# Kernel optimization log

Measured on AMD Instinct MI355X. Metric: run time of the kernel, lower is better.

The kernel has to match this reference:

```python
import jax, jax.numpy as jnp
import numpy as np

WINDOW = 32  # hardcoded in module; half-window = 16

def _final_mask(T):
    # sparse local window |i-j| <= 16 AND causal j <= i  =>  0 <= i-j <= 16
    i = jnp.arange(T)[:, None]
    j = jnp.arange(T)[None, :]
    d = i - j
    return (d >= 0) & (d <= WINDOW // 2)  # [T, T] bool

def setup_inputs() -> dict:
    key = jax.random.key(0)
    k1, k2, k3, k4 = jax.random.split(key, 4)
    B, T, C, H = 2, 8192, 1024, 64
    x = jax.random.normal(k1, (B, T, C), dtype=jnp.float32)
    Wq = jax.random.normal(k2, (C, H), dtype=jnp.float32) * (1.0 / np.sqrt(C))
    Wk = jax.random.normal(k3, (C, H), dtype=jnp.float32) * (1.0 / np.sqrt(C))
    Wv = jax.random.normal(k4, (C, H), dtype=jnp.float32) * (1.0 / np.sqrt(C))
    return {"x": x, "Wq": Wq, "Wk": Wk, "Wv": Wv}

def reference(x, Wq, Wk, Wv):
    B, T, C = x.shape
    H = Wq.shape[1]
    scale = jnp.sqrt(jnp.float32(H))
    q = jnp.einsum('btc,ch->bth', x, Wq)
    k = jnp.einsum('btc,ch->bth', x, Wk)
    v = jnp.einsum('btc,ch->bth', x, Wv)
    scores = jnp.einsum('bth,bsh->bts', q, k) / scale  # [B, T, T]
    mask = _final_mask(T)  # [T, T]
    scores = jnp.where(mask[None, :, :], scores, -jnp.inf)
    attn = jax.nn.softmax(scores, axis=-1)  # dropout is identity in eval mode
    out = jnp.einsum('bts,bsh->bth', attn, v)  # [B, T, H]
    return out
```

## Files before the change

kernel.cpp:

```cpp
#include <hip/hip_runtime.h>

typedef __bf16 bf16x8 __attribute__((ext_vector_type(8)));
typedef float f32x4 __attribute__((ext_vector_type(4)));

#define T_SEQ 8192
#define NB 2
#define CDIM 1024
#define HDIM 64
#define NROWS (NB * T_SEQ)

static __device__ __forceinline__ unsigned short f2b(float f) {
    union { float f; unsigned u; } a; a.f = f;
    unsigned r = a.u + 0x7FFFu + ((a.u >> 16) & 1u);
    return (unsigned short)(r >> 16);
}

__global__ __launch_bounds__(256) void wt_kernel(const float* __restrict__ Wq,
                                                 const float* __restrict__ Wk,
                                                 const float* __restrict__ Wv,
                                                 unsigned short* __restrict__ WT) {
    int idx = blockIdx.x * 256 + threadIdx.x;
    int m   = idx >> 16;
    int rem = idx & 65535;
    int n = rem >> 10, k = rem & 1023;
    const float* W = (m == 0) ? Wq : (m == 1) ? Wk : Wv;
    WT[idx] = f2b(W[k * HDIM + n]);
}

__global__ __launch_bounds__(256) void qkv_kernel(const float* __restrict__ x,
                                                  const unsigned short* __restrict__ WT,
                                                  float* __restrict__ q,
                                                  float* __restrict__ k,
                                                  float* __restrict__ v) {
    __shared__ unsigned short Al[32][72];
    __shared__ unsigned short Bl[192][72];

    int tid  = threadIdx.x;
    int lane = tid & 63;
    int w    = tid >> 6;
    int lr   = lane & 15, lg = lane >> 4;
    long row0 = (long)blockIdx.x * 32;

    f32x4 acc[2][3];
    #pragma unroll
    for (int mi = 0; mi < 2; ++mi)
        #pragma unroll
        for (int ni = 0; ni < 3; ++ni)
            acc[mi][ni] = (f32x4){0.f, 0.f, 0.f, 0.f};

    int ar = tid >> 3, aq = tid & 7;
    const float* xr = x + (row0 + ar) * CDIM;

    for (int kt = 0; kt < CDIM; kt += 64) {
        float4 f0 = ((const float4*)(xr + kt))[aq];
        float4 f1 = ((const float4*)(xr + kt))[aq + 8];
        ushort4 u0, u1;
        u0.x = f2b(f0.x); u0.y = f2b(f0.y); u0.z = f2b(f0.z); u0.w = f2b(f0.w);
        u1.x = f2b(f1.x); u1.y = f2b(f1.y); u1.z = f2b(f1.z); u1.w = f2b(f1.w);
        *(ushort4*)&Al[ar][aq * 4]      = u0;
        *(ushort4*)&Al[ar][32 + aq * 4] = u1;

        #pragma unroll
        for (int i = 0; i < 6; ++i) {
            int wi = tid + i * 256;
            int r = wi >> 3, ch = wi & 7;
            uint4 val = *(const uint4*)(WT + r * CDIM + kt + ch * 8);
            *(uint4*)&Bl[r][ch * 8] = val;
        }
        __syncthreads();

        #pragma unroll
        for (int kk = 0; kk < 2; ++kk) {
            bf16x8 a0 = *(const bf16x8*)&Al[lr][kk * 32 + lg * 8];
            bf16x8 a1 = *(const bf16x8*)&Al[16 + lr][kk * 32 + lg * 8];
            bf16x8 b0 = *(const bf16x8*)&Bl[w * 48 + lr][kk * 32 + lg * 8];
            bf16x8 b1 = *(const bf16x8*)&Bl[w * 48 + 16 + lr][kk * 32 + lg * 8];
            bf16x8 b2 = *(const bf16x8*)&Bl[w * 48 + 32 + lr][kk * 32 + lg * 8];
            acc[0][0] = __builtin_amdgcn_mfma_f32_16x16x32_bf16(a0, b0, acc[0][0], 0, 0, 0);
            acc[1][0] = __builtin_amdgcn_mfma_f32_16x16x32_bf16(a1, b0, acc[1][0], 0, 0, 0);
            acc[0][1] = __builtin_amdgcn_mfma_f32_16x16x32_bf16(a0, b1, acc[0][1], 0, 0, 0);
            acc[1][1] = __builtin_amdgcn_mfma_f32_16x16x32_bf16(a1, b1, acc[1][1], 0, 0, 0);
            acc[0][2] = __builtin_amdgcn_mfma_f32_16x16x32_bf16(a0, b2, acc[0][2], 0, 0, 0);
            acc[1][2] = __builtin_amdgcn_mfma_f32_16x16x32_bf16(a1, b2, acc[1][2], 0, 0, 0);
        }
        __syncthreads();
    }

    #pragma unroll
    for (int mi = 0; mi < 2; ++mi)
        #pragma unroll
        for (int ni = 0; ni < 3; ++ni) {
            int cg  = w * 48 + ni * 16 + lr;
            int mat = cg >> 6, cc = cg & 63;
            float* op = (mat == 0) ? q : (mat == 1) ? k : v;
            long rbase = row0 + mi * 16 + lg * 4;
            #pragma unroll
            for (int j = 0; j < 4; ++j)
                op[(rbase + j) * HDIM + cc] = acc[mi][ni][j];
        }
}

#define DOT4(a, b) ((a).x*(b).x + (a).y*(b).y + (a).z*(b).z + (a).w*(b).w)

__global__ __launch_bounds__(256) void attn_kernel(const float* __restrict__ q,
                                                   const float* __restrict__ k,
                                                   const float* __restrict__ v,
                                                   float* __restrict__ out) {
    __shared__ float Kl[80][68];
    __shared__ float Vl[80][68];
    __shared__ float Ql[64][68];

    int tid = threadIdx.x;
    int b   = blockIdx.y;
    int r0  = blockIdx.x * 64;
    const float* qb = q + (long)b * T_SEQ * HDIM;
    const float* kb = k + (long)b * T_SEQ * HDIM;
    const float* vb = v + (long)b * T_SEQ * HDIM;

    #pragma unroll
    for (int i = 0; i < 5; ++i) {
        int f = tid + i * 256;
        int r = f >> 4, c = (f & 15) * 4;
        int gr = r0 - 16 + r; if (gr < 0) gr = 0;
        *(float4*)&Kl[r][c] = *(const float4*)(kb + (long)gr * HDIM + c);
        *(float4*)&Vl[r][c] = *(const float4*)(vb + (long)gr * HDIM + c);
    }
    #pragma unroll
    for (int i = 0; i < 4; ++i) {
        int f = tid + i * 256;
        int r = f >> 4, c = (f & 15) * 4;
        *(float4*)&Ql[r][c] = *(const float4*)(qb + (long)(r0 + r) * HDIM + c);
    }
    __syncthreads();

    int r = tid >> 2, p = tid & 3;
    int i_row = r0 + r;

    float4 q0 = *(float4*)&Ql[r][p * 16 + 0];
    float4 q1 = *(float4*)&Ql[r][p * 16 + 4];
    float4 q2 = *(float4*)&Ql[r][p * 16 + 8];
    float4 q3 = *(float4*)&Ql[r][p * 16 + 12];

    float s[17];
    float mx = -1e30f;
    #pragma unroll
    for (int jj = 0; jj < 17; ++jj) {
        float d;
        if (i_row - 16 + jj < 0) {
            d = -1e30f;
        } else {
            const float* kr = &Kl[r + jj][p * 16];
            float4 k0 = *(const float4*)(kr + 0);
            float4 k1 = *(const float4*)(kr + 4);
            float4 k2 = *(const float4*)(kr + 8);
            float4 k3 = *(const float4*)(kr + 12);
            float pd = DOT4(q0, k0) + DOT4(q1, k1) + DOT4(q2, k2) + DOT4(q3, k3);
            pd += __shfl_xor(pd, 1, 64);
            pd += __shfl_xor(pd, 2, 64);
            d = pd * 0.125f;
        }
        s[jj] = d;
        mx = fmaxf(mx, d);
    }

    float denom = 0.f;
    float4 o0 = {0,0,0,0}, o1 = {0,0,0,0}, o2 = {0,0,0,0}, o3 = {0,0,0,0};
    #pragma unroll
    for (int jj = 0; jj < 17; ++jj) {
        float wgt = expf(s[jj] - mx);
        denom += wgt;
        const float* vr = &Vl[r + jj][p * 16];
        float4 v0 = *(const float4*)(vr + 0);
        float4 v1 = *(const float4*)(vr + 4);
        float4 v2 = *(const float4*)(vr + 8);
        float4 v3 = *(const float4*)(vr + 12);
        o0.x += wgt * v0.x; o0.y += wgt * v0.y; o0.z += wgt * v0.z; o0.w += wgt * v0.w;
        o1.x += wgt * v1.x; o1.y += wgt * v1.y; o1.z += wgt * v1.z; o1.w += wgt * v1.w;
        o2.x += wgt * v2.x; o2.y += wgt * v2.y; o2.z += wgt * v2.z; o2.w += wgt * v2.w;
        o3.x += wgt * v3.x; o3.y += wgt * v3.y; o3.z += wgt * v3.z; o3.w += wgt * v3.w;
    }
    float inv = 1.f / denom;
    o0.x *= inv; o0.y *= inv; o0.z *= inv; o0.w *= inv;
    o1.x *= inv; o1.y *= inv; o1.z *= inv; o1.w *= inv;
    o2.x *= inv; o2.y *= inv; o2.z *= inv; o2.w *= inv;
    o3.x *= inv; o3.y *= inv; o3.z *= inv; o3.w *= inv;

    float* ob = out + ((long)b * T_SEQ + i_row) * HDIM + p * 16;
    *(float4*)&ob[0]  = o0;
    *(float4*)&ob[4]  = o1;
    *(float4*)&ob[8]  = o2;
    *(float4*)&ob[12] = o3;
}

extern "C" void kernel_launch(void* const* d_in, const int* in_sizes, int n_in,
                              void* d_out, int out_size, void* d_ws, size_t ws_size,
                              hipStream_t stream) {
    const float* x  = (const float*)d_in[0];
    const float* Wq = (const float*)d_in[1];
    const float* Wk = (const float*)d_in[2];
    const float* Wv = (const float*)d_in[3];
    float* out = (float*)d_out;

    unsigned short* WT = (unsigned short*)d_ws;
    float* qws = (float*)((char*)d_ws + 393216);
    float* kws = qws + (long)NROWS * HDIM;
    float* vws = kws + (long)NROWS * HDIM;

    wt_kernel<<<dim3(768), dim3(256), 0, stream>>>(Wq, Wk, Wv, WT);
    qkv_kernel<<<dim3(NROWS / 32), dim3(256), 0, stream>>>(x, WT, qws, kws, vws);
    attn_kernel<<<dim3(T_SEQ / 64, NB), dim3(256), 0, stream>>>(qws, kws, vws, out);
}
```

Before: 125.6 us.

## Drop LDS staging in QKV GEMM and attention; load operands directly from global

The QKV projection kernel no longer stages x and W tiles in shared memory with block barriers. Each wave computes 16 rows by all 192 output columns, reading bf16 weight fragments directly from global/L2 and software-prefetching the next x slice. The attention kernel reads Q, K and V straight from global memory instead of copying a window into LDS, skips masked rows, and uses fast __expf. This removes LDS traffic and synchronization, but it relies on cache hits for the redundant weight and K/V reads across waves and gives up LDS reuse.

Result: slower. 200.0 us (+59.3%).

```diff
diff --git a/kernel.cpp b/kernel.cpp
--- a/kernel.cpp
+++ b/kernel.cpp
@@ -13,6 +13,13 @@
     union { float f; unsigned u; } a; a.f = f;
     unsigned r = a.u + 0x7FFFu + ((a.u >> 16) & 1u);
     return (unsigned short)(r >> 16);
+}
+
+static __device__ __forceinline__ bf16x8 pack8(float4 a, float4 b) {
+    union { bf16x8 v; unsigned short u[8]; } r;
+    r.u[0] = f2b(a.x); r.u[1] = f2b(a.y); r.u[2] = f2b(a.z); r.u[3] = f2b(a.w);
+    r.u[4] = f2b(b.x); r.u[5] = f2b(b.y); r.u[6] = f2b(b.z); r.u[7] = f2b(b.w);
+    return r.v;
 }
 
 __global__ __launch_bounds__(256) void wt_kernel(const float* __restrict__ Wq,
@@ -32,72 +39,45 @@
                                                   float* __restrict__ q,
                                                   float* __restrict__ k,
                                                   float* __restrict__ v) {
-    __shared__ unsigned short Al[32][72];
-    __shared__ unsigned short Bl[192][72];
-
     int tid  = threadIdx.x;
     int lane = tid & 63;
     int w    = tid >> 6;
     int lr   = lane & 15, lg = lane >> 4;
-    long row0 = (long)blockIdx.x * 32;
+    long r0  = ((long)blockIdx.x * 4 + w) * 16;
 
-    f32x4 acc[2][3];
+    const float* xrow = x + (r0 + lr) * CDIM + lg * 8;
+    const unsigned short* bbase = WT + (long)lr * CDIM + lg * 8;
+
+    f32x4 acc[12];
     #pragma unroll
-    for (int mi = 0; mi < 2; ++mi)
+    for (int ni = 0; ni < 12; ++ni) acc[ni] = (f32x4){0.f, 0.f, 0.f, 0.f};
+
+    float4 c0 = *(const float4*)(xrow + 0);
+    float4 c1 = *(const float4*)(xrow + 4);
+
+    for (int ks = 0; ks < CDIM; ks += 32) {
+        int kn = (ks + 32) & (CDIM - 1);
+        float4 n0 = *(const float4*)(xrow + kn + 0);
+        float4 n1 = *(const float4*)(xrow + kn + 4);
+        bf16x8 af = pack8(c0, c1);
         #pragma unroll
-        for (int ni = 0; ni < 3; ++ni)
-            acc[mi][ni] = (f32x4){0.f, 0.f, 0.f, 0.f};
-
-    int ar = tid >> 3, aq = tid & 7;
-    const float* xr = x + (row0 + ar) * CDIM;
-
-    for (int kt = 0; kt < CDIM; kt += 64) {
-        float4 f0 = ((const float4*)(xr + kt))[aq];
-        float4 f1 = ((const float4*)(xr + kt))[aq + 8];
-        ushort4 u0, u1;
-        u0.x = f2b(f0.x); u0.y = f2b(f0.y); u0.z = f2b(f0.z); u0.w = f2b(f0.w);
-        u1.x = f2b(f1.x); u1.y = f2b(f1.y); u1.z = f2b(f1.z); u1.w = f2b(f1.w);
-        *(ushort4*)&Al[ar][aq * 4]      = u0;
-        *(ushort4*)&Al[ar][32 + aq * 4] = u1;
-
-        #pragma unroll
-        for (int i = 0; i < 6; ++i) {
-            int wi = tid + i * 256;
-            int r = wi >> 3, ch = wi & 7;
-            uint4 val = *(const uint4*)(WT + r * CDIM + kt + ch * 8);
-            *(uint4*)&Bl[r][ch * 8] = val;
+        for (int ni = 0; ni < 12; ++ni) {
+            bf16x8 bf = *(const bf16x8*)(bbase + ni * 16 * CDIM + ks);
+            acc[ni] = __builtin_amdgcn_mfma_f32_16x16x32_bf16(af, bf, acc[ni], 0, 0, 0);
         }
-        __syncthreads();
-
-        #pragma unroll
-        for (int kk = 0; kk < 2; ++kk) {
-            bf16x8 a0 = *(const bf16x8*)&Al[lr][kk * 32 + lg * 8];
-            bf16x8 a1 = *(const bf16x8*)&Al[16 + lr][kk * 32 + lg * 8];
-            bf16x8 b0 = *(const bf16x8*)&Bl[w * 48 + lr][kk * 32 + lg * 8];
-            bf16x8 b1 = *(const bf16x8*)&Bl[w * 48 + 16 + lr][kk * 32 + lg * 8];
-            bf16x8 b2 = *(const bf16x8*)&Bl[w * 48 + 32 + lr][kk * 32 + lg * 8];
-            acc[0][0] = __builtin_amdgcn_mfma_f32_16x16x32_bf16(a0, b0, acc[0][0], 0, 0, 0);
-            acc[1][0] = __builtin_amdgcn_mfma_f32_16x16x32_bf16(a1, b0, acc[1][0], 0, 0, 0);
-            acc[0][1] = __builtin_amdgcn_mfma_f32_16x16x32_bf16(a0, b1, acc[0][1], 0, 0, 0);
-            acc[1][1] = __builtin_amdgcn_mfma_f32_16x16x32_bf16(a1, b1, acc[1][1], 0, 0, 0);
-            acc[0][2] = __builtin_amdgcn_mfma_f32_16x16x32_bf16(a0, b2, acc[0][2], 0, 0, 0);
-            acc[1][2] = __builtin_amdgcn_mfma_f32_16x16x32_bf16(a1, b2, acc[1][2], 0, 0, 0);
-        }
-        __syncthreads();
+        c0 = n0; c1 = n1;
     }
 
     #pragma unroll
-    for (int mi = 0; mi < 2; ++mi)
+    for (int ni = 0; ni < 12; ++ni) {
+        int cg  = ni * 16 + lr;
+        int mat = cg >> 6, cc = cg & 63;
+        float* op = (mat == 0) ? q : (mat == 1) ? k : v;
+        long rbase = r0 + lg * 4;
         #pragma unroll
-        for (int ni = 0; ni < 3; ++ni) {
-            int cg  = w * 48 + ni * 16 + lr;
-            int mat = cg >> 6, cc = cg & 63;
-            float* op = (mat == 0) ? q : (mat == 1) ? k : v;
-            long rbase = row0 + mi * 16 + lg * 4;
-            #pragma unroll
-            for (int j = 0; j < 4; ++j)
-                op[(rbase + j) * HDIM + cc] = acc[mi][ni][j];
-        }
+        for (int j = 0; j < 4; ++j)
+            op[(rbase + j) * HDIM + cc] = acc[ni][j];
+    }
 }
 
 #define DOT4(a, b) ((a).x*(b).x + (a).y*(b).y + (a).z*(b).z + (a).w*(b).w)
@@ -106,50 +86,31 @@
                                                    const float* __restrict__ k,
                                                    const float* __restrict__ v,
                                                    float* __restrict__ out) {
-    __shared__ float Kl[80][68];
-    __shared__ float Vl[80][68];
-    __shared__ float Ql[64][68];
-
     int tid = threadIdx.x;
     int b   = blockIdx.y;
     int r0  = blockIdx.x * 64;
-    const float* qb = q + (long)b * T_SEQ * HDIM;
+    int r   = tid >> 2, p = tid & 3;
+    int i_row = r0 + r;
+
+    const float* qb = q + ((long)b * T_SEQ + i_row) * HDIM + p * 16;
     const float* kb = k + (long)b * T_SEQ * HDIM;
     const float* vb = v + (long)b * T_SEQ * HDIM;
 
-    #pragma unroll
-    for (int i = 0; i < 5; ++i) {
-        int f = tid + i * 256;
-        int r = f >> 4, c = (f & 15) * 4;
-        int gr = r0 - 16 + r; if (gr < 0) gr = 0;
-        *(float4*)&Kl[r][c] = *(const float4*)(kb + (long)gr * HDIM + c);
-        *(float4*)&Vl[r][c] = *(const float4*)(vb + (long)gr * HDIM + c);
-    }
-    #pragma unroll
-    for (int i = 0; i < 4; ++i) {
-        int f = tid + i * 256;
-        int r = f >> 4, c = (f & 15) * 4;
-        *(float4*)&Ql[r][c] = *(const float4*)(qb + (long)(r0 + r) * HDIM + c);
-    }
-    __syncthreads();
-
-    int r = tid >> 2, p = tid & 3;
-    int i_row = r0 + r;
-
-    float4 q0 = *(float4*)&Ql[r][p * 16 + 0];
-    float4 q1 = *(float4*)&Ql[r][p * 16 + 4];
-    float4 q2 = *(float4*)&Ql[r][p * 16 + 8];
-    float4 q3 = *(float4*)&Ql[r][p * 16 + 12];
+    float4 q0 = *(const float4*)(qb + 0);
+    float4 q1 = *(const float4*)(qb + 4);
+    float4 q2 = *(const float4*)(qb + 8);
+    float4 q3 = *(const float4*)(qb + 12);
 
     float s[17];
     float mx = -1e30f;
     #pragma unroll
     for (int jj = 0; jj < 17; ++jj) {
+        int j_row = i_row - 16 + jj;
         float d;
-        if (i_row - 16 + jj < 0) {
+        if (j_row < 0) {
             d = -1e30f;
         } else {
-            const float* kr = &Kl[r + jj][p * 16];
+            const float* kr = kb + (long)j_row * HDIM + p * 16;
             float4 k0 = *(const float4*)(kr + 0);
             float4 k1 = *(const float4*)(kr + 4);
             float4 k2 = *(const float4*)(kr + 8);
@@ -167,9 +128,11 @@
     float4 o0 = {0,0,0,0}, o1 = {0,0,0,0}, o2 = {0,0,0,0}, o3 = {0,0,0,0};
     #pragma unroll
     for (int jj = 0; jj < 17; ++jj) {
-        float wgt = expf(s[jj] - mx);
+        int j_row = i_row - 16 + jj;
+        if (j_row < 0) continue;
+        float wgt = __expf(s[jj] - mx);
         denom += wgt;
-        const float* vr = &Vl[r + jj][p * 16];
+        const float* vr = vb + (long)j_row * HDIM + p * 16;
         float4 v0 = *(const float4*)(vr + 0);
         float4 v1 = *(const float4*)(vr + 4);
         float4 v2 = *(const float4*)(vr + 8);
@@ -207,6 +170,6 @@
     float* vws = kws + (long)NROWS * HDIM;
 
     wt_kernel<<<dim3(768), dim3(256), 0, stream>>>(Wq, Wk, Wv, WT);
-    qkv_kernel<<<dim3(NROWS / 32), dim3(256), 0, stream>>>(x, WT, qws, kws, vws);
+    qkv_kernel<<<dim3(NROWS / 64), dim3(256), 0, stream>>>(x, WT, qws, kws, vws);
     attn_kernel<<<dim3(T_SEQ / 64, NB), dim3(256), 0, stream>>>(qws, kws, vws, out);
 }
```
